# Kernel optimization log

Measured on AMD Instinct MI355X. Metric: run time of the kernel, lower is better.

Reference implementation:

```python
import jax, jax.numpy as jnp
import numpy as np

P = 64       # number of pathways
NV = 512     # features per pathway (nvar[i])
W = 256      # hidden width per pathway
COV = 16     # covariates
B = 2048     # batch
EPS = 1e-5   # BatchNorm eps
SLOPE = 0.2  # LeakyReLU negative slope


def _lrelu(v):
    return jnp.where(v >= 0, v, SLOPE * v)


def setup_inputs() -> dict:
    key = jax.random.key(0)
    ks = jax.random.split(key, 8)
    x = jax.random.normal(ks[0], (B, P * NV + COV), dtype=jnp.float32)
    # per-pathway weights (no bias), stacked across pathways -> grouped GEMM
    W1 = jax.random.normal(ks[1], (P, NV, W), dtype=jnp.float32) * (1.0 / np.sqrt(NV))
    W2 = jax.random.normal(ks[2], (P, W, W), dtype=jnp.float32) * (1.0 / np.sqrt(W))
    W3 = jax.random.normal(ks[3], (P, W), dtype=jnp.float32) * (1.0 / np.sqrt(W))
    gamma = jnp.ones((P,), dtype=jnp.float32)   # bn_path weight
    beta = jnp.zeros((P,), dtype=jnp.float32)   # bn_path bias
    fc_w = jax.random.normal(ks[4], (P + COV, 1), dtype=jnp.float32) * 0.05
    fc_b = jnp.full((1,), 0.001, dtype=jnp.float32)
    return {"x": x, "W1": W1, "W2": W2, "W3": W3,
            "gamma": gamma, "beta": beta, "fc_w": fc_w, "fc_b": fc_b}


def reference(x, W1, W2, W3, gamma, beta, fc_w, fc_b):
    # pathway blocks (dropout = identity in eval): grouped GEMMs over P pathways
    xp = x[:, : P * NV].reshape(B, P, NV)
    h = _lrelu(jnp.einsum('bpi,pio->bpo', xp, W1))
    h = _lrelu(jnp.einsum('bpi,pio->bpo', h, W2))
    p = _lrelu(jnp.einsum('bpi,pi->bp', h, W3))          # [B, P]
    # BatchNorm1d (training-mode batch statistics, biased variance)
    mean = p.mean(axis=0)
    var = p.var(axis=0)
    pn = (p - mean) / jnp.sqrt(var + EPS) * gamma + beta
    # global L2 (Frobenius) normalization, as torch.norm(pathway_layer, 2)
    pn = pn / jnp.linalg.norm(pn)
    # concat covariates, final linear + sigmoid
    z = jnp.concatenate([pn, x[:, P * NV: P * NV + COV]], axis=1)  # [B, P+COV]
    return jax.nn.sigmoid(z @ fc_w + fc_b)                         # [B, 1]
```

## Files before the change

kernel.cpp:

```cpp
#include <hip/hip_runtime.h>
#include <hip/hip_bf16.h>

#define PW 64
#define NV 512
#define HW 256
#define COV 16
#define BATCH 2048
#define XROW (PW * NV + COV)
#define IMG 16384
#define AIMG 4096

typedef short s16x8 __attribute__((ext_vector_type(8)));
typedef float f32x4 __attribute__((ext_vector_type(4)));

__device__ __forceinline__ unsigned short f2bf(float f) {
    union { float f; unsigned int u; } v;
    v.f = f;
    unsigned int u = v.u;
    unsigned int r = (u + 0x7fffu + ((u >> 16) & 1u)) >> 16;
    return (unsigned short)r;
}

__device__ __forceinline__ unsigned int pack2(float a, float b) {
    __hip_bfloat162 h = __float22bfloat162_rn(float2{a, b});
    union { __hip_bfloat162 h; unsigned int u; } c;
    c.h = h;
    return c.u;
}

__device__ __forceinline__ float lrelu(float v) { return v >= 0.f ? v : 0.2f * v; }

__device__ __forceinline__ void gl_lds16(const void* g, void* l) {
    __builtin_amdgcn_global_load_lds(
        (const __attribute__((address_space(1))) void*)g,
        (__attribute__((address_space(3))) void*)l, 16, 0, 0);
}

__global__ __launch_bounds__(256)
void transpose_all(const float* __restrict__ W1, const float* __restrict__ W2,
                   unsigned short* __restrict__ W1I, unsigned short* __restrict__ W2I) {
    __shared__ float tile[64][260];
    int bx = blockIdx.x;
    const float* src;
    unsigned short* dst;
    if (bx < 512) {
        int p = bx >> 3, kb = bx & 7;
        src = W1 + ((size_t)p * NV + kb * 64) * HW;
        dst = W1I + (size_t)(p * 8 + kb) * IMG;
    } else {
        bx -= 512;
        int p = bx >> 2, kb = bx & 3;
        src = W2 + ((size_t)p * HW + kb * 64) * HW;
        dst = W2I + (size_t)(p * 4 + kb) * IMG;
    }
    const int t = threadIdx.x;
    #pragma unroll
    for (int i = 0; i < 16; ++i) {
        int idx = t + i * 256;
        int r = idx >> 6, c4 = (idx & 63) << 2;
        *(float4*)&tile[r][c4] = *(const float4*)(src + (size_t)r * HW + c4);
    }
    __syncthreads();
    #pragma unroll
    for (int pass = 0; pass < 8; ++pass) {
        int idx = pass * 256 + t;
        int n = idx >> 3, s = idx & 7;
        int g = s ^ (n & 7);
        unsigned short v[8];
        #pragma unroll
        for (int j = 0; j < 8; ++j)
            v[j] = f2bf(tile[g * 8 + j][n]);
        *(s16x8*)(dst + (size_t)idx * 8) = *(s16x8*)v;
    }
}

__global__ __launch_bounds__(256, 2)
void gemm1(const float* __restrict__ x, const unsigned short* __restrict__ W1I,
           unsigned short* __restrict__ H1I) {
    __shared__ __align__(16) unsigned short As[2][64 * 64];
    __shared__ __align__(16) unsigned short Bs[2][256 * 64];

    const int lin = blockIdx.x;
    const int xcd = lin & 7;
    const int idx = lin >> 3;
    const int p   = xcd * 8 + (idx >> 5);
    const int m   = idx & 31;
    const int bm0 = m * 64;

    const int t = threadIdx.x;
    const int lane = t & 63;
    const int wave = t >> 6;
    const int wn   = wave * 64;
    const int l15  = lane & 15;
    const int quad = lane >> 4;

    const float* Ap          = x   + (size_t)p * NV;
    const unsigned short* B1 = W1I + (size_t)p * 8 * IMG;

    int arow[4], acol[4], aoff[4];
    #pragma unroll
    for (int i = 0; i < 4; ++i) {
        int ii = t + i * 256;
        arow[i] = ii >> 4;
        acol[i] = (ii & 15) * 4;
        int slot = (acol[i] >> 3) ^ (arow[i] & 7);
        aoff[i] = arow[i] * 64 + slot * 8 + (acol[i] & 7);
    }

    float4 aA[4], aB[4];

#define XLOAD(dst, k0) { \
    _Pragma("unroll") \
    for (int i = 0; i < 4; ++i) \
        dst[i] = *(const float4*)(Ap + (size_t)(bm0 + arow[i]) * XROW + (k0) + acol[i]); }

#define APACK(src, buf) { \
    _Pragma("unroll") \
    for (int i = 0; i < 4; ++i) { \
        uint2 u; \
        u.x = pack2(src[i].x, src[i].y); \
        u.y = pack2(src[i].z, src[i].w); \
        *(uint2*)&As[buf][aoff[i]] = u; } }

#define B1STAGE(buf, kb) { \
    const unsigned short* img = B1 + (size_t)(kb) * IMG; \
    _Pragma("unroll") \
    for (int c = 0; c < 8; ++c) { \
        int off = wave * 8192 + c * 1024; \
        gl_lds16((const char*)img + off + lane * 16, (char*)Bs[buf] + off); } }

#define MFMA1(buf) { \
    _Pragma("unroll") \
    for (int kk = 0; kk < 64; kk += 32) { \
        s16x8 af[4], bfr[4]; \
        _Pragma("unroll") \
        for (int mi = 0; mi < 4; ++mi) { \
            int row = mi * 16 + l15; \
            int slot = ((kk >> 3) + quad) ^ (row & 7); \
            af[mi] = *(const s16x8*)&As[buf][row * 64 + slot * 8]; } \
        _Pragma("unroll") \
        for (int ni = 0; ni < 4; ++ni) { \
            int row = wn + ni * 16 + l15; \
            int slot = ((kk >> 3) + quad) ^ (row & 7); \
            bfr[ni] = *(const s16x8*)&Bs[buf][row * 64 + slot * 8]; } \
        _Pragma("unroll") \
        for (int mi = 0; mi < 4; ++mi) \
            _Pragma("unroll") \
            for (int ni = 0; ni < 4; ++ni) \
                acc[mi][ni] = __builtin_amdgcn_mfma_f32_16x16x32_bf16( \
                    af[mi], bfr[ni], acc[mi][ni], 0, 0, 0); } }

    XLOAD(aA, 0);
    B1STAGE(0, 0);
    APACK(aA, 0);
    XLOAD(aA, 64);
    __syncthreads();

    f32x4 acc[4][4] = {};

    #pragma unroll
    for (int s2 = 0; s2 < 4; ++s2) {
        const int te = 2 * s2;
        if (te + 1 < 8) B1STAGE((te + 1) & 1, te + 1);
        if (te + 2 < 8) XLOAD(aB, (te + 2) * 64);
        MFMA1(te & 1);
        if (te + 1 < 8) APACK(aA, (te + 1) & 1);
        __syncthreads();
        const int to = te + 1;
        if (to + 1 < 8) B1STAGE((to + 1) & 1, to + 1);
        if (to + 2 < 8) XLOAD(aA, (to + 2) * 64);
        MFMA1(to & 1);
        if (to + 1 < 8) APACK(aB, (to + 1) & 1);
        __syncthreads();
    }

    unsigned short* Hp = H1I + ((size_t)(p * 32 + m) * 4 + wave) * AIMG;
    #pragma unroll
    for (int mi = 0; mi < 4; ++mi)
        #pragma unroll
        for (int ni = 0; ni < 4; ++ni)
            #pragma unroll
            for (int r = 0; r < 4; ++r) {
                int row = mi * 16 + quad * 4 + r;
                int col = ni * 16 + l15;
                int slot = (col >> 3) ^ (row & 7);
                Hp[row * 64 + slot * 8 + (col & 7)] = f2bf(lrelu(acc[mi][ni][r]));
            }
#undef XLOAD
#undef APACK
#undef B1STAGE
#undef MFMA1
}

__global__ __launch_bounds__(256, 2)
void gemm2(const unsigned short* __restrict__ H1I, const unsigned short* __restrict__ W2I,
           const float* __restrict__ W3, float* __restrict__ pvec) {
    __shared__ __align__(16) unsigned short As[2][64 * 64];
    __shared__ __align__(16) unsigned short Bs[2][256 * 64];

    const int lin = blockIdx.x;
    const int xcd = lin & 7;
    const int idx = lin >> 3;
    const int p   = xcd * 8 + (idx >> 5);
    const int m   = idx & 31;
    const int bm0 = m * 64;

    const int t = threadIdx.x;
    const int lane = t & 63;
    const int wave = t >> 6;
    const int wn   = wave * 64;
    const int l15  = lane & 15;
    const int quad = lane >> 4;

    const unsigned short* Aimg = H1I + (size_t)(p * 32 + m) * 4 * AIMG;
    const unsigned short* B2   = W2I + (size_t)p * 4 * IMG;

#define A2STAGE(buf, kb) { \
    const unsigned short* img = Aimg + (size_t)(kb) * AIMG; \
    _Pragma("unroll") \
    for (int c = 0; c < 2; ++c) { \
        int off = wave * 2048 + c * 1024; \
        gl_lds16((const char*)img + off + lane * 16, (char*)As[buf] + off); } }

#define B2STAGE(buf, kb) { \
    const unsigned short* img = B2 + (size_t)(kb) * IMG; \
    _Pragma("unroll") \
    for (int c = 0; c < 8; ++c) { \
        int off = wave * 8192 + c * 1024; \
        gl_lds16((const char*)img + off + lane * 16, (char*)Bs[buf] + off); } }

#define MFMA2(buf) { \
    _Pragma("unroll") \
    for (int kk = 0; kk < 64; kk += 32) { \
        s16x8 af[4], bfr[4]; \
        _Pragma("unroll") \
        for (int mi = 0; mi < 4; ++mi) { \
            int row = mi * 16 + l15; \
            int slot = ((kk >> 3) + quad) ^ (row & 7); \
            af[mi] = *(const s16x8*)&As[buf][row * 64 + slot * 8]; } \
        _Pragma("unroll") \
        for (int ni = 0; ni < 4; ++ni) { \
            int row = wn + ni * 16 + l15; \
            int slot = ((kk >> 3) + quad) ^ (row & 7); \
            bfr[ni] = *(const s16x8*)&Bs[buf][row * 64 + slot * 8]; } \
        _Pragma("unroll") \
        for (int mi = 0; mi < 4; ++mi) \
            _Pragma("unroll") \
            for (int ni = 0; ni < 4; ++ni) \
                acc[mi][ni] = __builtin_amdgcn_mfma_f32_16x16x32_bf16( \
                    af[mi], bfr[ni], acc[mi][ni], 0, 0, 0); } }

    A2STAGE(0, 0);
    B2STAGE(0, 0);
    __syncthreads();

    f32x4 acc[4][4] = {};
    #pragma unroll
    for (int t4 = 0; t4 < 4; ++t4) {
        if (t4 + 1 < 4) { A2STAGE((t4 + 1) & 1, t4 + 1); B2STAGE((t4 + 1) & 1, t4 + 1); }
        MFMA2(t4 & 1);
        __syncthreads();
    }
#undef A2STAGE
#undef B2STAGE
#undef MFMA2

    float* red = (float*)&As[0][0];
    float w3v[4];
    #pragma unroll
    for (int ni = 0; ni < 4; ++ni)
        w3v[ni] = W3[(size_t)p * HW + wn + ni * 16 + l15];
    float part[4][4];
    #pragma unroll
    for (int mi = 0; mi < 4; ++mi) {
        #pragma unroll
        for (int r = 0; r < 4; ++r) {
            float s = 0.f;
            #pragma unroll
            for (int ni = 0; ni < 4; ++ni)
                s += lrelu(acc[mi][ni][r]) * w3v[ni];
            part[mi][r] = s;
        }
    }
    #pragma unroll
    for (int off = 1; off < 16; off <<= 1)
        #pragma unroll
        for (int mi = 0; mi < 4; ++mi)
            #pragma unroll
            for (int r = 0; r < 4; ++r)
                part[mi][r] += __shfl_xor(part[mi][r], off);
    if (l15 == 0)
        #pragma unroll
        for (int mi = 0; mi < 4; ++mi)
            #pragma unroll
            for (int r = 0; r < 4; ++r)
                red[wave * 64 + mi * 16 + quad * 4 + r] = part[mi][r];
    __syncthreads();
    if (t < 64) {
        float s = red[0 * 64 + t] + red[1 * 64 + t] + red[2 * 64 + t] + red[3 * 64 + t];
        pvec[(size_t)p * BATCH + bm0 + t] = lrelu(s);
    }
}

__global__ __launch_bounds__(256)
void stats_k(const float* __restrict__ pvec, float* __restrict__ stat) {
    const int p = blockIdx.x;
    float s = 0.f, q = 0.f;
    for (int i = threadIdx.x; i < BATCH; i += 256) {
        float v = pvec[(size_t)p * BATCH + i];
        s += v; q += v * v;
    }
    #pragma unroll
    for (int off = 32; off; off >>= 1) {
        s += __shfl_down(s, off);
        q += __shfl_down(q, off);
    }
    __shared__ float ls[4], lq[4];
    const int wave = threadIdx.x >> 6, lane = threadIdx.x & 63;
    if (lane == 0) { ls[wave] = s; lq[wave] = q; }
    __syncthreads();
    if (threadIdx.x == 0) {
        float S = ls[0] + ls[1] + ls[2] + ls[3];
        float Q = lq[0] + lq[1] + lq[2] + lq[3];
        float mean = S * (1.f / BATCH);
        float var  = Q * (1.f / BATCH) - mean * mean;
        stat[p]       = mean;
        stat[64 + p]  = rsqrtf(var + 1e-5f);
        stat[128 + p] = var;
    }
}

__global__ __launch_bounds__(256)
void final_k(const float* __restrict__ pvec, const float* __restrict__ stat,
             const float* __restrict__ gamma, const float* __restrict__ beta,
             const float* __restrict__ x, const float* __restrict__ fc_w,
             const float* __restrict__ fc_b, float* __restrict__ out) {
    const int b = blockIdx.x * 256 + threadIdx.x;
    float nsq = 0.f;
    #pragma unroll
    for (int p = 0; p < PW; ++p) {
        float g = gamma[p], bt = beta[p], var = stat[128 + p], inv = stat[64 + p];
        nsq += (float)BATCH * (g * g * var * inv * inv + bt * bt);
    }
    const float rn = rsqrtf(nsq);
    float acc = fc_b[0];
    #pragma unroll
    for (int p = 0; p < PW; ++p) {
        float pn = (pvec[(size_t)p * BATCH + b] - stat[p]) * stat[64 + p] * gamma[p] + beta[p];
        acc += pn * rn * fc_w[p];
    }
    #pragma unroll
    for (int c = 0; c < COV; ++c)
        acc += x[(size_t)b * XROW + PW * NV + c] * fc_w[PW + c];
    out[b] = 1.f / (1.f + __expf(-acc));
}

extern "C" void kernel_launch(void* const* d_in, const int* in_sizes, int n_in,
                              void* d_out, int out_size, void* d_ws, size_t ws_size,
                              hipStream_t stream) {
    const float* x     = (const float*)d_in[0];
    const float* W1    = (const float*)d_in[1];
    const float* W2    = (const float*)d_in[2];
    const float* W3    = (const float*)d_in[3];
    const float* gamma = (const float*)d_in[4];
    const float* beta  = (const float*)d_in[5];
    const float* fc_w  = (const float*)d_in[6];
    const float* fc_b  = (const float*)d_in[7];
    float* out = (float*)d_out;

    char* ws = (char*)d_ws;
    size_t off = 0;
    unsigned short* W1I = (unsigned short*)(ws + off); off += (size_t)PW * NV * HW * 2;
    unsigned short* W2I = (unsigned short*)(ws + off); off += (size_t)PW * HW * HW * 2;
    unsigned short* H1I = (unsigned short*)(ws + off); off += (size_t)PW * BATCH * HW * 2;
    float* pvec = (float*)(ws + off); off += (size_t)PW * BATCH * 4;
    float* stat = (float*)(ws + off); off += 256 * 4;

    transpose_all<<<dim3(512 + 256), 256, 0, stream>>>(W1, W2, W1I, W2I);

    gemm1<<<dim3(2048), 256, 0, stream>>>(x, W1I, H1I);

    gemm2<<<dim3(2048), 256, 0, stream>>>(H1I, W2I, W3, pvec);

    stats_k<<<PW, 256, 0, stream>>>(pvec, stat);

    final_k<<<BATCH / 256, 256, 0, stream>>>(pvec, stat, gamma, beta, x, fc_w, fc_b, out);
}
```

Before: 509.4 us.

## Fuse both pathway GEMMs into one kernel keeping hidden activations in LDS

Merges gemm1 and gemm2 into a single kernel. The 64x256 bf16 hidden tile stays in shared memory and feeds the second GEMM directly, which removes the global write and read of the H1 intermediate and one kernel launch. W2 is re-laid out into 32-wide K slices so that its double-buffered staging fits alongside the resident hidden tile in a single 80KB LDS allocation. The change also adds s_setprio around the MFMA blocks. The larger LDS footprint per block may limit occupancy, and the second GEMM now uses smaller K steps with more barriers.

```diff
diff --git a/kernel.cpp b/kernel.cpp
--- a/kernel.cpp
+++ b/kernel.cpp
@@ -8,7 +8,7 @@
 #define BATCH 2048
 #define XROW (PW * NV + COV)
 #define IMG 16384
-#define AIMG 4096
+#define IMG2 8192
 
 typedef short s16x8 __attribute__((ext_vector_type(8)));
 typedef float f32x4 __attribute__((ext_vector_type(4)));
@@ -41,19 +41,17 @@
                    unsigned short* __restrict__ W1I, unsigned short* __restrict__ W2I) {
     __shared__ float tile[64][260];
     int bx = blockIdx.x;
+    const int t = threadIdx.x;
+    const bool isW1 = bx < 512;
     const float* src;
-    unsigned short* dst;
-    if (bx < 512) {
+    if (isW1) {
         int p = bx >> 3, kb = bx & 7;
         src = W1 + ((size_t)p * NV + kb * 64) * HW;
-        dst = W1I + (size_t)(p * 8 + kb) * IMG;
     } else {
-        bx -= 512;
-        int p = bx >> 2, kb = bx & 3;
-        src = W2 + ((size_t)p * HW + kb * 64) * HW;
-        dst = W2I + (size_t)(p * 4 + kb) * IMG;
-    }
-    const int t = threadIdx.x;
+        int b2 = bx - 512;
+        int p = b2 >> 2, kb64 = b2 & 3;
+        src = W2 + ((size_t)p * HW + kb64 * 64) * HW;
+    }
     #pragma unroll
     for (int i = 0; i < 16; ++i) {
         int idx = t + i * 256;
@@ -61,24 +59,46 @@
         *(float4*)&tile[r][c4] = *(const float4*)(src + (size_t)r * HW + c4);
     }
     __syncthreads();
-    #pragma unroll
-    for (int pass = 0; pass < 8; ++pass) {
-        int idx = pass * 256 + t;
-        int n = idx >> 3, s = idx & 7;
-        int g = s ^ (n & 7);
-        unsigned short v[8];
-        #pragma unroll
-        for (int j = 0; j < 8; ++j)
-            v[j] = f2bf(tile[g * 8 + j][n]);
-        *(s16x8*)(dst + (size_t)idx * 8) = *(s16x8*)v;
+    if (isW1) {
+        int p = bx >> 3, kb = bx & 7;
+        unsigned short* dst = W1I + (size_t)(p * 8 + kb) * IMG;
+        #pragma unroll
+        for (int pass = 0; pass < 8; ++pass) {
+            int idx = pass * 256 + t;
+            int n = idx >> 3, s = idx & 7;
+            int g = s ^ (n & 7);
+            unsigned short v[8];
+            #pragma unroll
+            for (int j = 0; j < 8; ++j)
+                v[j] = f2bf(tile[g * 8 + j][n]);
+            *(s16x8*)(dst + (size_t)idx * 8) = *(s16x8*)v;
+        }
+    } else {
+        int b2 = bx - 512;
+        int p = b2 >> 2, kb64 = b2 & 3;
+        unsigned short* dst = W2I + (size_t)(p * 8 + kb64 * 2) * IMG2;
+        #pragma unroll
+        for (int pass = 0; pass < 8; ++pass) {
+            int idx = pass * 256 + t;
+            int h = idx >> 10;
+            int rem = idx & 1023;
+            int n = rem >> 2, s = rem & 3;
+            int g = s ^ ((n >> 1) & 3);
+            int krow = h * 32 + g * 8;
+            unsigned short v[8];
+            #pragma unroll
+            for (int j = 0; j < 8; ++j)
+                v[j] = f2bf(tile[krow + j][n]);
+            *(s16x8*)(dst + (size_t)h * IMG2 + n * 32 + s * 8) = *(s16x8*)v;
+        }
     }
 }
 
 __global__ __launch_bounds__(256, 2)
-void gemm1(const float* __restrict__ x, const unsigned short* __restrict__ W1I,
-           unsigned short* __restrict__ H1I) {
-    __shared__ __align__(16) unsigned short As[2][64 * 64];
-    __shared__ __align__(16) unsigned short Bs[2][256 * 64];
+void pathway_fused(const float* __restrict__ x, const unsigned short* __restrict__ W1I,
+                   const unsigned short* __restrict__ W2I, const float* __restrict__ W3,
+                   float* __restrict__ pvec) {
+    __shared__ __align__(16) unsigned short lds[40960];
 
     const int lin = blockIdx.x;
     const int xcd = lin & 7;
@@ -96,6 +116,7 @@
 
     const float* Ap          = x   + (size_t)p * NV;
     const unsigned short* B1 = W1I + (size_t)p * 8 * IMG;
+    const unsigned short* B2 = W2I + (size_t)p * 8 * IMG2;
 
     int arow[4], acol[4], aoff[4];
     #pragma unroll
@@ -107,7 +128,8 @@
         aoff[i] = arow[i] * 64 + slot * 8 + (acol[i] & 7);
     }
 
-    float4 aA[4], aB[4];
+    float4 S0[4], S1[4];
+    f32x4 acc[4][4] = {};
 
 #define XLOAD(dst, k0) { \
     _Pragma("unroll") \
@@ -115,21 +137,25 @@
         dst[i] = *(const float4*)(Ap + (size_t)(bm0 + arow[i]) * XROW + (k0) + acol[i]); }
 
 #define APACK(src, buf) { \
+    unsigned short* Asb = lds + 32768 + (buf) * 4096; \
     _Pragma("unroll") \
     for (int i = 0; i < 4; ++i) { \
         uint2 u; \
         u.x = pack2(src[i].x, src[i].y); \
         u.y = pack2(src[i].z, src[i].w); \
-        *(uint2*)&As[buf][aoff[i]] = u; } }
+        *(uint2*)&Asb[aoff[i]] = u; } }
 
 #define B1STAGE(buf, kb) { \
     const unsigned short* img = B1 + (size_t)(kb) * IMG; \
     _Pragma("unroll") \
     for (int c = 0; c < 8; ++c) { \
         int off = wave * 8192 + c * 1024; \
-        gl_lds16((const char*)img + off + lane * 16, (char*)Bs[buf] + off); } }
-
-#define MFMA1(buf) { \
+        gl_lds16((const char*)img + off + lane * 16, (char*)lds + (buf) * 32768 + off); } }
+
+#define MFMA_A(buf) { \
+    const unsigned short* Asb = lds + 32768 + (buf) * 4096; \
+    const unsigned short* Bsb = lds + (buf) * 16384; \
+    __builtin_amdgcn_s_setprio(1); \
     _Pragma("unroll") \
     for (int kk = 0; kk < 64; kk += 32) { \
         s16x8 af[4], bfr[4]; \
@@ -137,135 +163,106 @@
         for (int mi = 0; mi < 4; ++mi) { \
             int row = mi * 16 + l15; \
             int slot = ((kk >> 3) + quad) ^ (row & 7); \
-            af[mi] = *(const s16x8*)&As[buf][row * 64 + slot * 8]; } \
+            af[mi] = *(const s16x8*)&Asb[row * 64 + slot * 8]; } \
         _Pragma("unroll") \
         for (int ni = 0; ni < 4; ++ni) { \
             int row = wn + ni * 16 + l15; \
             int slot = ((kk >> 3) + quad) ^ (row & 7); \
-            bfr[ni] = *(const s16x8*)&Bs[buf][row * 64 + slot * 8]; } \
+            bfr[ni] = *(const s16x8*)&Bsb[row * 64 + slot * 8]; } \
         _Pragma("unroll") \
         for (int mi = 0; mi < 4; ++mi) \
             _Pragma("unroll") \
             for (int ni = 0; ni < 4; ++ni) \
                 acc[mi][ni] = __builtin_amdgcn_mfma_f32_16x16x32_bf16( \
-                    af[mi], bfr[ni], acc[mi][ni], 0, 0, 0); } }
-
-    XLOAD(aA, 0);
-    B1STAGE(0, 0);
-    APACK(aA, 0);
-    XLOAD(aA, 64);
-    __syncthreads();
-
-    f32x4 acc[4][4] = {};
-
-    #pragma unroll
-    for (int s2 = 0; s2 < 4; ++s2) {
-        const int te = 2 * s2;
-        if (te + 1 < 8) B1STAGE((te + 1) & 1, te + 1);
-        if (te + 2 < 8) XLOAD(aB, (te + 2) * 64);
-        MFMA1(te & 1);
-        if (te + 1 < 8) APACK(aA, (te + 1) & 1);
-        __syncthreads();
-        const int to = te + 1;
-        if (to + 1 < 8) B1STAGE((to + 1) & 1, to + 1);
-        if (to + 2 < 8) XLOAD(aA, (to + 2) * 64);
-        MFMA1(to & 1);
-        if (to + 1 < 8) APACK(aB, (to + 1) & 1);
-        __syncthreads();
-    }
-
-    unsigned short* Hp = H1I + ((size_t)(p * 32 + m) * 4 + wave) * AIMG;
-    #pragma unroll
-    for (int mi = 0; mi < 4; ++mi)
-        #pragma unroll
-        for (int ni = 0; ni < 4; ++ni)
-            #pragma unroll
-            for (int r = 0; r < 4; ++r) {
-                int row = mi * 16 + quad * 4 + r;
-                int col = ni * 16 + l15;
-                int slot = (col >> 3) ^ (row & 7);
-                Hp[row * 64 + slot * 8 + (col & 7)] = f2bf(lrelu(acc[mi][ni][r]));
-            }
-#undef XLOAD
-#undef APACK
-#undef B1STAGE
-#undef MFMA1
-}
-
-__global__ __launch_bounds__(256, 2)
-void gemm2(const unsigned short* __restrict__ H1I, const unsigned short* __restrict__ W2I,
-           const float* __restrict__ W3, float* __restrict__ pvec) {
-    __shared__ __align__(16) unsigned short As[2][64 * 64];
-    __shared__ __align__(16) unsigned short Bs[2][256 * 64];
-
-    const int lin = blockIdx.x;
-    const int xcd = lin & 7;
-    const int idx = lin >> 3;
-    const int p   = xcd * 8 + (idx >> 5);
-    const int m   = idx & 31;
-    const int bm0 = m * 64;
-
-    const int t = threadIdx.x;
-    const int lane = t & 63;
-    const int wave = t >> 6;
-    const int wn   = wave * 64;
-    const int l15  = lane & 15;
-    const int quad = lane >> 4;
-
-    const unsigned short* Aimg = H1I + (size_t)(p * 32 + m) * 4 * AIMG;
-    const unsigned short* B2   = W2I + (size_t)p * 4 * IMG;
-
-#define A2STAGE(buf, kb) { \
-    const unsigned short* img = Aimg + (size_t)(kb) * AIMG; \
-    _Pragma("unroll") \
-    for (int c = 0; c < 2; ++c) { \
-        int off = wave * 2048 + c * 1024; \
-        gl_lds16((const char*)img + off + lane * 16, (char*)As[buf] + off); } }
-
-#define B2STAGE(buf, kb) { \
-    const unsigned short* img = B2 + (size_t)(kb) * IMG; \
-    _Pragma("unroll") \
-    for (int c = 0; c < 8; ++c) { \
-        int off = wave * 8192 + c * 1024; \
-        gl_lds16((const char*)img + off + lane * 16, (char*)Bs[buf] + off); } }
-
-#define MFMA2(buf) { \
-    _Pragma("unroll") \
-    for (int kk = 0; kk < 64; kk += 32) { \
+                    af[mi], bfr[ni], acc[mi][ni], 0, 0, 0); } \
+    __builtin_amdgcn_s_setprio(0); }
+
+#define W2STAGE(buf, kb) { \
+    const unsigned short* img = B2 + (size_t)(kb) * IMG2; \
+    _Pragma("unroll") \
+    for (int c = 0; c < 4; ++c) { \
+        int off = wave * 4096 + c * 1024; \
+        gl_lds16((const char*)img + off + lane * 16, (char*)lds + 32768 + (buf) * 16384 + off); } }
+
+#define MFMA_B(buf, kb) { \
+    const unsigned short* W2b = lds + 16384 + (buf) * 8192; \
+    __builtin_amdgcn_s_setprio(1); \
+    { \
         s16x8 af[4], bfr[4]; \
         _Pragma("unroll") \
         for (int mi = 0; mi < 4; ++mi) { \
             int row = mi * 16 + l15; \
-            int slot = ((kk >> 3) + quad) ^ (row & 7); \
-            af[mi] = *(const s16x8*)&As[buf][row * 64 + slot * 8]; } \
+            int slot = ((kb) * 4 + quad) ^ (row & 7); \
+            af[mi] = *(const s16x8*)&lds[row * 256 + slot * 8]; } \
         _Pragma("unroll") \
         for (int ni = 0; ni < 4; ++ni) { \
             int row = wn + ni * 16 + l15; \
-            int slot = ((kk >> 3) + quad) ^ (row & 7); \
-            bfr[ni] = *(const s16x8*)&Bs[buf][row * 64 + slot * 8]; } \
+            int slot = quad ^ ((row >> 1) & 3); \
+            bfr[ni] = *(const s16x8*)&W2b[row * 32 + slot * 8]; } \
         _Pragma("unroll") \
         for (int mi = 0; mi < 4; ++mi) \
             _Pragma("unroll") \
             for (int ni = 0; ni < 4; ++ni) \
                 acc[mi][ni] = __builtin_amdgcn_mfma_f32_16x16x32_bf16( \
-                    af[mi], bfr[ni], acc[mi][ni], 0, 0, 0); } }
-
-    A2STAGE(0, 0);
-    B2STAGE(0, 0);
-    __syncthreads();
-
-    f32x4 acc[4][4] = {};
-    #pragma unroll
-    for (int t4 = 0; t4 < 4; ++t4) {
-        if (t4 + 1 < 4) { A2STAGE((t4 + 1) & 1, t4 + 1); B2STAGE((t4 + 1) & 1, t4 + 1); }
-        MFMA2(t4 & 1);
+                    af[mi], bfr[ni], acc[mi][ni], 0, 0, 0); \
+    } \
+    __builtin_amdgcn_s_setprio(0); }
+
+    XLOAD(S0, 0);
+    B1STAGE(0, 0);
+    APACK(S0, 0);
+    XLOAD(S0, 64);
+    __syncthreads();
+
+    #pragma unroll
+    for (int s2 = 0; s2 < 4; ++s2) {
+        const int te = 2 * s2;
+        if (te + 1 < 8) B1STAGE(1, te + 1);
+        if (te + 1 < 8) APACK(S0, 1);
+        if (te + 2 < 8) XLOAD(S1, (te + 2) * 64);
+        MFMA_A(0);
         __syncthreads();
-    }
-#undef A2STAGE
-#undef B2STAGE
-#undef MFMA2
-
-    float* red = (float*)&As[0][0];
+        const int to = te + 1;
+        if (to + 1 < 8) B1STAGE(0, to + 1);
+        if (to + 1 < 8) APACK(S1, 0);
+        if (to + 2 < 8) XLOAD(S0, (to + 2) * 64);
+        MFMA_A(1);
+        __syncthreads();
+    }
+
+    #pragma unroll
+    for (int mi = 0; mi < 4; ++mi)
+        #pragma unroll
+        for (int ni = 0; ni < 4; ++ni)
+            #pragma unroll
+            for (int r = 0; r < 4; ++r) {
+                int row = mi * 16 + quad * 4 + r;
+                int col = wn + ni * 16 + l15;
+                int slot = (col >> 3) ^ (row & 7);
+                lds[row * 256 + slot * 8 + (col & 7)] = f2bf(lrelu(acc[mi][ni][r]));
+            }
+    W2STAGE(0, 0);
+    __syncthreads();
+
+    #pragma unroll
+    for (int mi = 0; mi < 4; ++mi)
+        #pragma unroll
+        for (int ni = 0; ni < 4; ++ni)
+            acc[mi][ni] = (f32x4){0.f, 0.f, 0.f, 0.f};
+
+    #pragma unroll
+    for (int s2 = 0; s2 < 4; ++s2) {
+        const int te = 2 * s2;
+        if (te + 1 < 8) W2STAGE(1, te + 1);
+        MFMA_B(0, te);
+        __syncthreads();
+        const int to = te + 1;
+        if (to + 1 < 8) W2STAGE(0, to + 1);
+        MFMA_B(1, to);
+        __syncthreads();
+    }
+
+    float* red = (float*)(lds + 32768);
     float w3v[4];
     #pragma unroll
     for (int ni = 0; ni < 4; ++ni)
@@ -300,6 +297,12 @@
         float s = red[0 * 64 + t] + red[1 * 64 + t] + red[2 * 64 + t] + red[3 * 64 + t];
         pvec[(size_t)p * BATCH + bm0 + t] = lrelu(s);
     }
+#undef XLOAD
+#undef APACK
+#undef B1STAGE
+#undef MFMA_A
+#undef W2STAGE
+#undef MFMA_B
 }
 
 __global__ __launch_bounds__(256)
@@ -372,15 +375,12 @@
     size_t off = 0;
     unsigned short* W1I = (unsigned short*)(ws + off); off += (size_t)PW * NV * HW * 2;
     unsigned short* W2I = (unsigned short*)(ws + off); off += (size_t)PW * HW * HW * 2;
-    unsigned short* H1I = (unsigned short*)(ws + off); off += (size_t)PW * BATCH * HW * 2;
     float* pvec = (float*)(ws + off); off += (size_t)PW * BATCH * 4;
     float* stat = (float*)(ws + off); off += 256 * 4;
 
     transpose_all<<<dim3(512 + 256), 256, 0, stream>>>(W1, W2, W1I, W2I);
 
-    gemm1<<<dim3(2048), 256, 0, stream>>>(x, W1I, H1I);
-
-    gemm2<<<dim3(2048), 256, 0, stream>>>(H1I, W2I, W3, pvec);
+    pathway_fused<<<dim3(2048), 256, 0, stream>>>(x, W1I, W2I, W3, pvec);
 
     stats_k<<<PW, 256, 0, stream>>>(pvec, stat);
 
```

Measured after the change: 488.1 us. -4.2%, faster.
